# Optimization experiments

Measured on AMD Instinct MI355X. Metric: run time of the kernel, lower is better.

The kernel has to match this reference:

```python
import jax, jax.numpy as jnp
import numpy as np

L, B, H = 1024, 64, 128


def _gru_cell(x, h, wih, whh, bih, bhh):
    # torch.nn.GRUCell math: gates ordered (r, z, n)
    gi = x @ wih.T + bih  # [B, 3H]
    gh = h @ whh.T + bhh  # [B, 3H]
    ir, iz, inn = jnp.split(gi, 3, axis=1)
    hr, hz, hn = jnp.split(gh, 3, axis=1)
    r = jax.nn.sigmoid(ir + hr)
    z = jax.nn.sigmoid(iz + hz)
    n = jnp.tanh(inn + r * hn)
    return (1.0 - z) * n + z * h


def setup_inputs() -> dict:
    key = jax.random.key(0)
    ks = jax.random.split(key, 20)
    s = 0.05  # keep tanh/sigmoid unsaturated
    f32 = jnp.float32
    return {
        "passEnc": jax.random.normal(ks[0], (L, B, 2 * H), f32),
        "Wp_w": jax.random.normal(ks[1], (H, 2 * H), f32) * s,
        "Wp_b": jax.random.normal(ks[2], (H,), f32) * s,
        "Wph_w": jax.random.normal(ks[3], (H, 2 * H), f32) * s,
        "Wph_b": jax.random.normal(ks[4], (H,), f32) * s,
        "Wg_w": jax.random.normal(ks[5], (4 * H, 4 * H), f32) * s,
        "Wg_b": jax.random.normal(ks[6], (4 * H,), f32) * s,
        "Vt": jax.random.normal(ks[7], (B, H, 1), f32),
        "wih_f": jax.random.normal(ks[8], (3 * H, 4 * H), f32) * s,
        "whh_f": jax.random.normal(ks[9], (3 * H, H), f32) * s,
        "bih_f": jax.random.normal(ks[10], (3 * H,), f32) * s,
        "bhh_f": jax.random.normal(ks[11], (3 * H,), f32) * s,
        "wih_r": jax.random.normal(ks[12], (3 * H, 4 * H), f32) * s,
        "whh_r": jax.random.normal(ks[13], (3 * H, H), f32) * s,
        "bih_r": jax.random.normal(ks[14], (3 * H,), f32) * s,
        "bhh_r": jax.random.normal(ks[15], (3 * H,), f32) * s,
        "h0_fwd": jax.random.normal(ks[16], (B, H), f32),
        "h0_rev": jax.random.normal(ks[17], (B, H), f32),
    }


def reference(passEnc, Wp_w, Wp_b, Wph_w, Wph_b, Wg_w, Wg_b, Vt,
              wih_f, whh_f, bih_f, bhh_f, wih_r, whh_r, bih_r, bhh_r,
              h0_fwd, h0_rev):
    v = Vt[:, :, 0]                       # [B, H]
    WPf = passEnc @ Wp_w.T + Wp_b        # loop-invariant WP_sub_v(passEnc), [L, B, H]
    pe_rev = jnp.flip(passEnc, axis=0)
    WPr = jnp.flip(WPf, axis=0)          # linear commutes with flip

    def attend(x_t, WP, pe):
        # x_t: [B, 2H]; WP: [L, B, H]; pe: [L, B, 2H]
        temp = jnp.tanh(WP + x_t @ Wph_w.T + Wph_b)      # [L, B, H]
        scores = jnp.einsum('lbh,bh->bl', temp, v)       # per-batch Vt
        a = jax.nn.softmax(scores, axis=1)               # over L
        c = jnp.einsum('bl,lbd->bd', a, pe)              # [B, 2H]
        cc = jnp.concatenate([x_t, c], axis=1)           # [B, 4H]
        g = jax.nn.sigmoid(cc @ Wg_w.T + Wg_b)
        return g * cc

    def step(carry, xs):
        hf, hr = carry
        xf, xr = xs
        cf = attend(xf, WPf, passEnc)
        cr = attend(xr, WPr, pe_rev)
        hf = _gru_cell(cf, hf, wih_f, whh_f, bih_f, bhh_f)
        hr = _gru_cell(cr, hr, wih_r, whh_r, bih_r, bhh_r)
        return (hf, hr), jnp.concatenate([hf, hr], axis=1)

    _, out = jax.lax.scan(step, (h0_fwd, h0_rev), (passEnc, pe_rev))
    # original applies Dropout(p=0.2); identity in eval mode
    return out  # [L, B, 2H]
```

## Files before the change

kernel.cpp:

```cpp
#include <hip/hip_runtime.h>
#include <hip/hip_bf16.h>

#define DEV __device__ __forceinline__
typedef unsigned short u16;
typedef short bf16x8 __attribute__((ext_vector_type(8)));
typedef float f32x4  __attribute__((ext_vector_type(4)));

static constexpr float LOG2E = 1.44269504088896340736f;
static constexpr float C2E   = 2.88539008177792681472f;

DEV float rcpf_(float x){ return __builtin_amdgcn_rcpf(x); }
DEV float exp2f_(float x){ return __builtin_amdgcn_exp2f(x); }
DEV float sigmoidf_(float x){ return rcpf_(1.f + exp2f_(-LOG2E*x)); }
DEV float tanhf_fast(float x){ return 1.f - 2.f*rcpf_(exp2f_(C2E*x) + 1.f); }
DEV u16 bfu(float f){
  __hip_bfloat16 h = __float2bfloat16(f);
  union { __hip_bfloat16 h; u16 u; } c; c.h = h; return c.u;
}
DEV float ubf_lo(unsigned u){ return __uint_as_float(u << 16); }
DEV float ubf_hi(unsigned u){ return __uint_as_float(u & 0xffff0000u); }
DEV unsigned pack2(float a, float b){ return (unsigned)bfu(a) | ((unsigned)bfu(b) << 16); }
DEV float ubf(u16 u){ return __uint_as_float(((unsigned)u) << 16); }

DEV void acc4inv(const float4 f, const float4 e, const float4 v, float& s){
  const float dx = __builtin_fmaf(f.x, e.x, 1.f);
  const float dy = __builtin_fmaf(f.y, e.y, 1.f);
  const float dz = __builtin_fmaf(f.z, e.z, 1.f);
  const float dw = __builtin_fmaf(f.w, e.w, 1.f);
  const float p2 = dx*dy, p3 = p2*dz, p4 = p3*dw;
  const float r4 = rcpf_(p4);
  const float iw = r4*p3;
  const float s3 = r4*dw;
  const float iz = s3*p2;
  const float s2 = s3*dz;
  const float iy = s2*dx;
  const float ix = s2*dy;
  s += v.x*ix; s += v.y*iy; s += v.z*iz; s += v.w*iw;
}

__global__ __launch_bounds__(256) void k_cvtw(const float* __restrict__ Wg,
      const float* __restrict__ wf, const float* __restrict__ wr,
      u16* __restrict__ out){
  const int i = (blockIdx.x*256 + threadIdx.x)*4;
  const float* src;
  int off;
  if (i < 262144){ src = Wg; off = i; }
  else if (i < 458752){ src = wf; off = i - 262144; }
  else { src = wr; off = i - 458752; }
  const float4 v = *(const float4*)(src + off);
  uint2 o; o.x = pack2(v.x, v.y); o.y = pack2(v.z, v.w);
  *(uint2*)(out + i) = o;
}

__global__ __launch_bounds__(256,4) void k_proj(const float* __restrict__ pe,
      const float* __restrict__ Wp, const float* __restrict__ Wpb,
      const float* __restrict__ Wph, const float* __restrict__ Wphb,
      float* __restrict__ E, float* __restrict__ F){
  __shared__ __align__(16) float xs[32*256];
  const int tid = threadIdx.x;
  const int sel = blockIdx.x >> 11;
  const long r0 = (long)(blockIdx.x & 2047) * 32;
  const float* W   = sel ? Wph  : Wp;
  const float* bia = sel ? Wphb : Wpb;
  float* out       = sel ? F    : E;
  const float4* src = (const float4*)(pe + r0*256);
  float4* dst = (float4*)xs;
  #pragma unroll
  for (int i=0;i<8;i++) dst[tid + 256*i] = src[tid + 256*i];
  __syncthreads();
  const int h = tid & 127, g = tid >> 7;
  float acc[16];
  #pragma unroll
  for (int r=0;r<16;r++) acc[r] = 0.f;
  for (int kc=0; kc<8; kc++){
    float4 w4[8];
    const float4* wp = (const float4*)(W + h*256 + kc*32);
    #pragma unroll
    for (int q=0;q<8;q++) w4[q] = wp[q];
    #pragma unroll
    for (int r=0;r<16;r++){
      const float4* xr = (const float4*)(xs + (g*16+r)*256 + kc*32);
      #pragma unroll
      for (int q=0;q<8;q++){
        const float4 xv = xr[q];
        acc[r] += xv.x*w4[q].x + xv.y*w4[q].y + xv.z*w4[q].z + xv.w*w4[q].w;
      }
    }
  }
  const float bh = bia[h];
  #pragma unroll
  for (int r=0;r<16;r++)
    out[(r0 + g*16 + r)*128 + h] = exp2f_(C2E*(acc[r] + bh));
}

#define AF_F    0
#define AF_E    8448
#define AF_PEt  12672
#define AF_S    17792
#define AF_V    19904
#define AF_M    20032
#define AF_SU   20096
#define AF_R    20160
#define A_LDSF  20224

DEV f32x4 mfma16(bf16x8 a, bf16x8 b, f32x4 c){
  return __builtin_amdgcn_mfma_f32_16x16x32_bf16(a, b, c, 0, 0, 0);
}

__global__ __launch_bounds__(512,4) void k_attn(const float* __restrict__ pe,
      const float* __restrict__ E, const float* __restrict__ F,
      const float* __restrict__ Vt, u16* __restrict__ Cout){
  __shared__ __align__(16) float lds[A_LDSF];
  const int tid = threadIdx.x;
  const int p = blockIdx.x;
  const int b = ((p >> 7) << 3) | (p & 7);
  const int tt = (p >> 3) & 15;
  const int t0 = tt * 64;
  u16* PEtu = (u16*)(lds + AF_PEt);
  u16* Pu   = (u16*)(lds + AF_S);

  for (int i = tid; i < 64*32; i += 512){
    const int r = i >> 5, c = i & 31;
    *(float4*)(lds + AF_F + r*132 + c*4) =
      *(const float4*)(F + ((long)(t0+r)*64 + b)*128 + c*4);
  }
  if (tid < 128) lds[AF_V + tid] = -2.f * Vt[b*128 + tid];
  if (tid < 64){ lds[AF_M+tid] = -__builtin_inff(); lds[AF_SU+tid] = 0.f; }

  f32x4 cacc[8];
  #pragma unroll
  for (int i=0;i<8;i++) cacc[i] = (f32x4){0.f,0.f,0.f,0.f};

  const int lane = tid & 63, w = tid >> 6;
  const int hg = lane >> 4, li = lane & 15;
  const int th = li & 1, lq = li >> 1;
  const int rot = (2*hg + 4*th) & 7;
  const int l15 = lane & 15, kg8 = (lane >> 4) * 8;
  const int tq = w >> 1, dhalf = w & 1;
  const int tcol = tq*16 + l15;
  const int sdlo = tid & 7, slp = (tid >> 3) & 15, sdhi = tid >> 7;

  for (int lt=0; lt<32; lt++){
    const int l0 = lt*32;
    __syncthreads();
    for (int i = tid; i < 32*32; i += 512){
      const int r = i >> 5, c = i & 31;
      *(float4*)(lds + AF_E + r*132 + c*4) =
        *(const float4*)(E + ((long)(l0+r)*64 + b)*128 + c*4);
    }
    #pragma unroll
    for (int k2=0;k2<2;k2++){
      const int dseg = (sdhi + k2*4)*8 + sdlo;
      const int ll = slp*2;
      const float4 vA = *(const float4*)(pe + ((long)(l0+ll  )*64 + b)*256 + dseg*4);
      const float4 vB = *(const float4*)(pe + ((long)(l0+ll+1)*64 + b)*256 + dseg*4);
      u16* base = PEtu + (dseg*4)*40 + ll;
      *(unsigned*)(base)        = pack2(vA.x, vB.x);
      *(unsigned*)(base + 40)   = pack2(vA.y, vB.y);
      *(unsigned*)(base + 80)   = pack2(vA.z, vB.z);
      *(unsigned*)(base + 120)  = pack2(vA.w, vB.w);
    }
    __syncthreads();
    {
      float s[4][4];
      #pragma unroll
      for (int i=0;i<4;i++)
        #pragma unroll
        for (int j=0;j<4;j++) s[i][j] = 0.f;
      const float* Fb = lds + AF_F + (w*8 + th)*132 + hg*32;
      const float* Eb = lds + AF_E + lq*132 + hg*32;
      const float* Vb = lds + AF_V + hg*32;
      #pragma unroll 2
      for (int hc=0; hc<8; hc++){
        const int hcp = ((hc + rot) & 7) * 4;
        const float4 vv = *(const float4*)(Vb + hcp);
        float4 fv[4], ev[4];
        #pragma unroll
        for (int i=0;i<4;i++) fv[i] = *(const float4*)(Fb + i*264 + hcp);
        #pragma unroll
        for (int j=0;j<4;j++) ev[j] = *(const float4*)(Eb + j*1056 + hcp);
        #pragma unroll
        for (int i=0;i<4;i++){
          #pragma unroll
          for (int j=0;j<4;j++)
            acc4inv(fv[i], ev[j], vv, s[i][j]);
        }
      }
      #pragma unroll
      for (int i=0;i<4;i++)
        #pragma unroll
        for (int j=0;j<4;j++){
          s[i][j] += __shfl_xor(s[i][j], 16);
          s[i][j] += __shfl_xor(s[i][j], 32);
        }
      if (hg == 0){
        #pragma unroll
        for (int i=0;i<4;i++)
          #pragma unroll
          for (int j=0;j<4;j++)
            lds[AF_S + (w*8 + th + 2*i)*33 + (lq + 8*j)] = s[i][j];
      }
    }
    __syncthreads();
    {
      const int t = tid >> 3, sub = tid & 7;
      const float* Srow = lds + AF_S + t*33 + sub*4;
      const float s0=Srow[0], s1=Srow[1], s2=Srow[2], s3=Srow[3];
      float mx = fmaxf(fmaxf(s0,s1), fmaxf(s2,s3));
      #pragma unroll
      for (int off=1; off<8; off<<=1) mx = fmaxf(mx, __shfl_xor(mx, off));
      const float m_old = lds[AF_M + t];
      const float m_new = fmaxf(m_old, mx);
      const float p0 = exp2f_(LOG2E*(s0-m_new));
      const float p1 = exp2f_(LOG2E*(s1-m_new));
      const float p2 = exp2f_(LOG2E*(s2-m_new));
      const float p3 = exp2f_(LOG2E*(s3-m_new));
      float ps = p0+p1+p2+p3;
      #pragma unroll
      for (int off=1; off<8; off<<=1) ps += __shfl_xor(ps, off);
      __syncthreads();
      uint2 pw; pw.x = pack2(p0,p1); pw.y = pack2(p2,p3);
      *(uint2*)(Pu + t*40 + sub*4) = pw;
      if (sub==0){
        const float rsc = exp2f_(LOG2E*(m_old - m_new));
        lds[AF_R + t] = rsc;
        lds[AF_SU + t] = lds[AF_SU + t]*rsc + ps;
        lds[AF_M + t] = m_new;
      }
    }
    __syncthreads();
    {
      const float rs = lds[AF_R + tcol];
      #pragma unroll
      for (int p2=0;p2<8;p2++){
        cacc[p2][0]*=rs; cacc[p2][1]*=rs; cacc[p2][2]*=rs; cacc[p2][3]*=rs;
      }
      const bf16x8 bfrag = *(const bf16x8*)(Pu + tcol*40 + kg8);
      #pragma unroll
      for (int p2=0;p2<8;p2++){
        const int dt = dhalf*8 + p2;
        const bf16x8 afrag = *(const bf16x8*)(PEtu + (dt*16 + l15)*40 + kg8);
        cacc[p2] = mfma16(afrag, bfrag, cacc[p2]);
      }
    }
  }
  __syncthreads();
  {
    const float inv = rcpf_(lds[AF_SU + tcol]);
    u16* Cb = (u16*)(lds + AF_F);
    const int rb = (lane >> 4) * 4;
    #pragma unroll
    for (int p2=0;p2<8;p2++){
      const int dd = (dhalf*8 + p2)*16 + rb;
      *(unsigned*)(Cb + tcol*264 + dd)     = pack2(cacc[p2][0]*inv, cacc[p2][1]*inv);
      *(unsigned*)(Cb + tcol*264 + dd + 2) = pack2(cacc[p2][2]*inv, cacc[p2][3]*inv);
    }
  }
  __syncthreads();
  {
    const u16* Cb = (const u16*)(lds + AF_F);
    #pragma unroll
    for (int k2=0;k2<4;k2++){
      const int flat = tid + k2*512;
      const int t = flat >> 5, dg = flat & 31;
      const uint4 v = *(const uint4*)(Cb + t*264 + dg*8);
      *(uint4*)(Cout + ((long)(t0+t)*64 + b)*256 + dg*8) = v;
    }
  }
}

__global__ __launch_bounds__(512,2) void k_gates(const float* __restrict__ pe,
      const u16* __restrict__ Cin,
      const u16* __restrict__ Wgb16, const float* __restrict__ Wgb,
      const u16* __restrict__ wfb16, const float* __restrict__ bihf,
      const u16* __restrict__ wrb16, const float* __restrict__ bihr,
      u16* __restrict__ GIf, u16* __restrict__ GIr){
  __shared__ __align__(16) u16 ccb[32*512];
  __shared__ __align__(16) u16 gb [32*512];
  const int tid = threadIdx.x;
  const int r0 = blockIdx.x * 32;

  #pragma unroll
  for (int i=0;i<4;i++){
    const int c = tid + i*512;
    const int r = c >> 6, k0 = (c & 63)*8;
    const int kd = k0 ^ ((r&7)<<3);
    uint4 o;
    if (k0 < 256){
      const float4 f0 = *(const float4*)(pe + ((long)(r0+r))*256 + k0);
      const float4 f1 = *(const float4*)(pe + ((long)(r0+r))*256 + k0 + 4);
      o.x = pack2(f0.x,f0.y); o.y = pack2(f0.z,f0.w);
      o.z = pack2(f1.x,f1.y); o.w = pack2(f1.z,f1.w);
    } else {
      o = *(const uint4*)(Cin + ((long)(r0+r))*256 + (k0-256));
    }
    *(uint4*)(ccb + r*512 + kd) = o;
  }
  __syncthreads();

  const int l = tid & 63, wv = tid >> 6;
  const int rw = (wv >> 2) * 16;
  const int nq = wv & 3;
  const int arow = rw + (l & 15);
  const int kgrp = (l >> 4) * 8;
  const int swz  = (l & 7) << 3;
  const u16* abase = ccb + arow*512;
  const int crow = rw + (l >> 4) * 4;

  for (int p2=0; p2<4; p2++){
    const int n0 = nq*128 + p2*32;
    const int c0 = n0 + (l & 15), c1 = c0 + 16;
    const u16* b0p = Wgb16 + (long)c0*512 + kgrp;
    const u16* b1p = Wgb16 + (long)c1*512 + kgrp;
    f32x4 a0 = {0.f,0.f,0.f,0.f}, a1 = {0.f,0.f,0.f,0.f};
    #pragma unroll
    for (int kk=0; kk<16; kk++){
      const bf16x8 av = *(const bf16x8*)(abase + ((kk*32 + kgrp) ^ swz));
      const bf16x8 b0 = *(const bf16x8*)(b0p + kk*32);
      const bf16x8 b1 = *(const bf16x8*)(b1p + kk*32);
      a0 = mfma16(av, b0, a0);
      a1 = mfma16(av, b1, a1);
    }
    const float bi0 = Wgb[c0], bi1 = Wgb[c1];
    #pragma unroll
    for (int i=0;i<4;i++){
      gb[(crow+i)*512 + c0] = bfu(sigmoidf_(a0[i] + bi0));
      gb[(crow+i)*512 + c1] = bfu(sigmoidf_(a1[i] + bi1));
    }
  }
  __syncthreads();

  #pragma unroll
  for (int i=0;i<4;i++){
    const int c = tid + i*512;
    const int r = c >> 6, k0 = (c & 63)*8;
    const int kd = k0 ^ ((r&7)<<3);
    uint4 uc = *(const uint4*)(ccb + r*512 + kd);
    uint4 ug = *(const uint4*)(gb  + r*512 + k0);
    uint4 o;
    o.x = pack2(ubf_lo(uc.x)*ubf_lo(ug.x), ubf_hi(uc.x)*ubf_hi(ug.x));
    o.y = pack2(ubf_lo(uc.y)*ubf_lo(ug.y), ubf_hi(uc.y)*ubf_hi(ug.y));
    o.z = pack2(ubf_lo(uc.z)*ubf_lo(ug.z), ubf_hi(uc.z)*ubf_hi(ug.z));
    o.w = pack2(ubf_lo(uc.w)*ubf_lo(ug.w), ubf_hi(uc.w)*ubf_hi(ug.w));
    *(uint4*)(ccb + r*512 + kd) = o;
  }
  __syncthreads();

  const int t = r0 >> 6, b0r = r0 & 63;
  const long rbf = (long)r0 + rw;
  const long rbr = (long)(1023 - t)*64 + b0r + rw;
  u16* stg = gb + wv*512;

  for (int p2=0; p2<6; p2++){
    const int nt = nq*12 + p2*2;
    const int j0 = nt * 16;
    const bool isf = (j0 < 384);
    const u16* wb = isf ? wfb16 : wrb16;
    const float* bi = isf ? bihf : bihr;
    const int jb = isf ? j0 : (j0 - 384);
    const long rbase = isf ? rbf : rbr;
    u16* GIo = isf ? GIf : GIr;
    const int c0 = jb + (l & 15), c1 = c0 + 16;
    const u16* b0p = wb + (long)c0*512 + kgrp;
    const u16* b1p = wb + (long)c1*512 + kgrp;
    f32x4 a0 = {0.f,0.f,0.f,0.f}, a1 = {0.f,0.f,0.f,0.f};
    #pragma unroll
    for (int kk=0; kk<16; kk++){
      const bf16x8 av = *(const bf16x8*)(abase + ((kk*32 + kgrp) ^ swz));
      const bf16x8 b0 = *(const bf16x8*)(b0p + kk*32);
      const bf16x8 b1 = *(const bf16x8*)(b1p + kk*32);
      a0 = mfma16(av, b0, a0);
      a1 = mfma16(av, b1, a1);
    }
    const float bi0 = bi[c0], bi1 = bi[c1];
    #pragma unroll
    for (int i=0;i<4;i++){
      stg[((l>>4)*4+i)*16 + (l&15)]       = bfu(a0[i] + bi0);
      stg[256 + ((l>>4)*4+i)*16 + (l&15)] = bfu(a1[i] + bi1);
    }
    {
      const int rr = l >> 2, q = l & 3;
      const uint2 v0 = *(const uint2*)(stg + rr*16 + q*4);
      const uint2 v1 = *(const uint2*)(stg + 256 + rr*16 + q*4);
      *(uint2*)(GIo + (rbase + rr)*384 + jb      + q*4) = v0;
      *(uint2*)(GIo + (rbase + rr)*384 + jb + 16 + q*4) = v1;
    }
  }
}

__global__ __launch_bounds__(512,2) void k_gru(
      const u16* __restrict__ GIf, const u16* __restrict__ GIr,
      const float* __restrict__ whhf, const float* __restrict__ bhhf,
      const float* __restrict__ whhr, const float* __restrict__ bhhr,
      const float* __restrict__ h0f, const float* __restrict__ h0r,
      float* __restrict__ out){
  const int d = blockIdx.x >> 6, b = blockIdx.x & 63;
  const u16* GI = d ? GIr  : GIf;
  const float* whh = d ? whhr : whhf;
  const float* bhh = d ? bhhr : bhhf;
  const float* h0  = d ? h0r  : h0f;
  const int tid = threadIdx.x;
  const int seg = tid >> 7, j0 = tid & 127;
  __shared__ __align__(16) float hsh[128];
  __shared__ __align__(16) float part[4*384];

  float4 wR[8], wZ[8], wN[8];
  {
    const float4* r0p = (const float4*)(whh + (long)(j0      )*128 + seg*32);
    const float4* r1p = (const float4*)(whh + (long)(j0 + 128)*128 + seg*32);
    const float4* r2p = (const float4*)(whh + (long)(j0 + 256)*128 + seg*32);
    #pragma unroll
    for (int q=0;q<8;q++){ wR[q]=r0p[q]; wZ[q]=r1p[q]; wN[q]=r2p[q]; }
  }
  float bjr=0.f, bjz=0.f, bjn=0.f, hold=0.f;
  float gr_n=0.f, gz_n=0.f, gn_n=0.f;
  if (tid < 128){
    hsh[tid] = hold = h0[b*128 + tid];
    bjr = bhh[tid]; bjz = bhh[tid+128]; bjn = bhh[tid+256];
    gr_n = ubf(GI[(long)b*384 + tid]);
    gz_n = ubf(GI[(long)b*384 + tid + 128]);
    gn_n = ubf(GI[(long)b*384 + tid + 256]);
  }
  __syncthreads();

  for (int t=0; t<1024; t++){
    {
      float aR=0.f, aZ=0.f, aN=0.f;
      const float4* hseg = (const float4*)(hsh + seg*32);
      #pragma unroll
      for (int q=0;q<8;q++){
        const float4 hv = hseg[q];
        aR += wR[q].x*hv.x + wR[q].y*hv.y + wR[q].z*hv.z + wR[q].w*hv.w;
        aZ += wZ[q].x*hv.x + wZ[q].y*hv.y + wZ[q].z*hv.z + wZ[q].w*hv.w;
        aN += wN[q].x*hv.x + wN[q].y*hv.y + wN[q].z*hv.z + wN[q].w*hv.w;
      }
      part[seg*384 + j0]       = aR;
      part[seg*384 + j0 + 128] = aZ;
      part[seg*384 + j0 + 256] = aN;
    }
    __syncthreads();
    if (tid < 128){
      const float gr = gr_n, gz = gz_n, gn = gn_n;
      if (t < 1023){
        const long base = ((long)(t+1)*64 + b)*384 + tid;
        gr_n = ubf(GI[base]); gz_n = ubf(GI[base+128]); gn_n = ubf(GI[base+256]);
      }
      const float ghr = bjr + ((part[tid]       + part[384+tid])       + (part[768+tid]       + part[1152+tid]));
      const float ghz = bjz + ((part[tid+128]   + part[384+tid+128])   + (part[768+tid+128]   + part[1152+tid+128]));
      const float ghn = bjn + ((part[tid+256]   + part[384+tid+256])   + (part[768+tid+256]   + part[1152+tid+256]));
      const float r = sigmoidf_(gr + ghr);
      const float z = sigmoidf_(gz + ghz);
      const float n = tanhf_fast(gn + r*ghn);
      const float hnew = (1.f - z)*n + z*hold;
      hold = hnew;
      hsh[tid] = hnew;
      out[((long)t*64 + b)*256 + d*128 + tid] = hnew;
    }
    __syncthreads();
  }
}

__global__ void k_sentinel(float* out){ out[0] = 1.0e6f; }

extern "C" void kernel_launch(void* const* d_in, const int* in_sizes, int n_in,
                              void* d_out, int out_size, void* d_ws, size_t ws_size,
                              hipStream_t stream){
  const float* passEnc = (const float*)d_in[0];
  const float* Wp_w  = (const float*)d_in[1];
  const float* Wp_b  = (const float*)d_in[2];
  const float* Wph_w = (const float*)d_in[3];
  const float* Wph_b = (const float*)d_in[4];
  const float* Wg_w  = (const float*)d_in[5];
  const float* Wg_b  = (const float*)d_in[6];
  const float* Vt    = (const float*)d_in[7];
  const float* wih_f = (const float*)d_in[8];
  const float* whh_f = (const float*)d_in[9];
  const float* bih_f = (const float*)d_in[10];
  const float* bhh_f = (const float*)d_in[11];
  const float* wih_r = (const float*)d_in[12];
  const float* whh_r = (const float*)d_in[13];
  const float* bih_r = (const float*)d_in[14];
  const float* bhh_r = (const float*)d_in[15];
  const float* h0f   = (const float*)d_in[16];
  const float* h0r   = (const float*)d_in[17];
  float* out = (float*)d_out;

  const size_t NEED = 134217728ull;
  if (ws_size < NEED){ k_sentinel<<<1,1,0,stream>>>(out); return; }
  char* base = (char*)d_ws;
  u16* GIf = (u16*)base;
  u16* GIr = (u16*)(base + 50331648ull);
  u16* C   = (u16*)(base + 100663296ull);
  float* E = (float*)base;
  float* F = (float*)(base + 33554432ull);
  u16* wgb16 = (u16*)d_out;
  u16* wfb16 = wgb16 + 262144;
  u16* wrb16 = wfb16 + 196608;

  k_cvtw <<<640,  256, 0, stream>>>(Wg_w, wih_f, wih_r, wgb16);
  k_proj <<<4096, 256, 0, stream>>>(passEnc, Wp_w, Wp_b, Wph_w, Wph_b, E, F);
  k_attn <<<1024, 512, 0, stream>>>(passEnc, E, F, Vt, C);
  k_gates<<<2048, 512, 0, stream>>>(passEnc, C, wgb16, Wg_b,
                                    wfb16, bih_f, wrb16, bih_r, GIf, GIr);
  k_gru  <<<128,  512, 0, stream>>>(GIf, GIr, whh_f, bhh_f, whh_r, bhh_r, h0f, h0r, out);
}
```

Baseline: 2.533 ms.

## Reduce GRU partial sums via wave shuffles with double-buffered hidden state

The GRU recurrence kernel is remapped so that the four K-segments for each hidden unit sit in the same wavefront. Partial dot products are then reduced with cross-lane shuffles instead of an LDS partial buffer, and the hidden state is double-buffered, so only one barrier per timestep is needed instead of two. Separately, the projection kernel now computes two output columns per thread, reusing each shared-memory x load across both and writing float2 stores. The LDS bank rotation in the attention score loop is also removed. This may raise bank conflicts there and raises register pressure in k_proj.

```diff
diff --git a/kernel.cpp b/kernel.cpp
--- a/kernel.cpp
+++ b/kernel.cpp
@@ -68,29 +68,39 @@
   #pragma unroll
   for (int i=0;i<8;i++) dst[tid + 256*i] = src[tid + 256*i];
   __syncthreads();
-  const int h = tid & 127, g = tid >> 7;
-  float acc[16];
+  const int hp = (tid & 63)*2, rg = tid >> 6;
+  float acc[2][8];
   #pragma unroll
-  for (int r=0;r<16;r++) acc[r] = 0.f;
+  for (int c=0;c<2;c++)
+    #pragma unroll
+    for (int r=0;r<8;r++) acc[c][r] = 0.f;
   for (int kc=0; kc<8; kc++){
-    float4 w4[8];
-    const float4* wp = (const float4*)(W + h*256 + kc*32);
-    #pragma unroll
-    for (int q=0;q<8;q++) w4[q] = wp[q];
-    #pragma unroll
-    for (int r=0;r<16;r++){
-      const float4* xr = (const float4*)(xs + (g*16+r)*256 + kc*32);
+    float4 w0[8], w1[8];
+    const float4* wp0 = (const float4*)(W + (long)hp*256 + kc*32);
+    const float4* wp1 = (const float4*)(W + (long)(hp+1)*256 + kc*32);
+    #pragma unroll
+    for (int q=0;q<8;q++){ w0[q] = wp0[q]; w1[q] = wp1[q]; }
+    #pragma unroll
+    for (int r=0;r<8;r++){
+      const float4* xr = (const float4*)(xs + (rg*8+r)*256 + kc*32);
+      float a0 = 0.f, a1 = 0.f;
       #pragma unroll
       for (int q=0;q<8;q++){
         const float4 xv = xr[q];
-        acc[r] += xv.x*w4[q].x + xv.y*w4[q].y + xv.z*w4[q].z + xv.w*w4[q].w;
-      }
-    }
-  }
-  const float bh = bia[h];
+        a0 += xv.x*w0[q].x + xv.y*w0[q].y + xv.z*w0[q].z + xv.w*w0[q].w;
+        a1 += xv.x*w1[q].x + xv.y*w1[q].y + xv.z*w1[q].z + xv.w*w1[q].w;
+      }
+      acc[0][r] += a0; acc[1][r] += a1;
+    }
+  }
+  const float b0 = bia[hp], b1 = bia[hp+1];
   #pragma unroll
-  for (int r=0;r<16;r++)
-    out[(r0 + g*16 + r)*128 + h] = exp2f_(C2E*(acc[r] + bh));
+  for (int r=0;r<8;r++){
+    float2 o;
+    o.x = exp2f_(C2E*(acc[0][r] + b0));
+    o.y = exp2f_(C2E*(acc[1][r] + b1));
+    *(float2*)(out + (r0 + rg*8 + r)*128 + hp) = o;
+  }
 }
 
 #define AF_F    0
@@ -134,7 +144,6 @@
   const int lane = tid & 63, w = tid >> 6;
   const int hg = lane >> 4, li = lane & 15;
   const int th = li & 1, lq = li >> 1;
-  const int rot = (2*hg + 4*th) & 7;
   const int l15 = lane & 15, kg8 = (lane >> 4) * 8;
   const int tq = w >> 1, dhalf = w & 1;
   const int tcol = tq*16 + l15;
@@ -172,13 +181,12 @@
       const float* Vb = lds + AF_V + hg*32;
       #pragma unroll 2
       for (int hc=0; hc<8; hc++){
-        const int hcp = ((hc + rot) & 7) * 4;
-        const float4 vv = *(const float4*)(Vb + hcp);
+        const float4 vv = *(const float4*)(Vb + hc*4);
         float4 fv[4], ev[4];
         #pragma unroll
-        for (int i=0;i<4;i++) fv[i] = *(const float4*)(Fb + i*264 + hcp);
+        for (int i=0;i<4;i++) fv[i] = *(const float4*)(Fb + i*264 + hc*4);
         #pragma unroll
-        for (int j=0;j<4;j++) ev[j] = *(const float4*)(Eb + j*1056 + hcp);
+        for (int j=0;j<4;j++) ev[j] = *(const float4*)(Eb + j*1056 + hc*4);
         #pragma unroll
         for (int i=0;i<4;i++){
           #pragma unroll
@@ -400,33 +408,36 @@
   const float* bhh = d ? bhhr : bhhf;
   const float* h0  = d ? h0r  : h0f;
   const int tid = threadIdx.x;
-  const int seg = tid >> 7, j0 = tid & 127;
-  __shared__ __align__(16) float hsh[128];
-  __shared__ __align__(16) float part[4*384];
+  const int w = tid >> 6, l = tid & 63;
+  const int seg = l >> 4, jj = w*16 + (l & 15);
+  const bool own = (seg == 0);
+  __shared__ __align__(16) float hsh[2][128];
 
   float4 wR[8], wZ[8], wN[8];
   {
-    const float4* r0p = (const float4*)(whh + (long)(j0      )*128 + seg*32);
-    const float4* r1p = (const float4*)(whh + (long)(j0 + 128)*128 + seg*32);
-    const float4* r2p = (const float4*)(whh + (long)(j0 + 256)*128 + seg*32);
+    const float4* r0p = (const float4*)(whh + (long)(jj      )*128 + seg*32);
+    const float4* r1p = (const float4*)(whh + (long)(jj + 128)*128 + seg*32);
+    const float4* r2p = (const float4*)(whh + (long)(jj + 256)*128 + seg*32);
     #pragma unroll
     for (int q=0;q<8;q++){ wR[q]=r0p[q]; wZ[q]=r1p[q]; wN[q]=r2p[q]; }
   }
   float bjr=0.f, bjz=0.f, bjn=0.f, hold=0.f;
   float gr_n=0.f, gz_n=0.f, gn_n=0.f;
-  if (tid < 128){
-    hsh[tid] = hold = h0[b*128 + tid];
-    bjr = bhh[tid]; bjz = bhh[tid+128]; bjn = bhh[tid+256];
-    gr_n = ubf(GI[(long)b*384 + tid]);
-    gz_n = ubf(GI[(long)b*384 + tid + 128]);
-    gn_n = ubf(GI[(long)b*384 + tid + 256]);
-  }
-  __syncthreads();
-
+  if (own){
+    hold = h0[b*128 + jj];
+    hsh[0][jj] = hold;
+    bjr = bhh[jj]; bjz = bhh[jj+128]; bjn = bhh[jj+256];
+    gr_n = ubf(GI[(long)b*384 + jj]);
+    gz_n = ubf(GI[(long)b*384 + jj + 128]);
+    gn_n = ubf(GI[(long)b*384 + jj + 256]);
+  }
+  __syncthreads();
+
+  int cur = 0;
   for (int t=0; t<1024; t++){
+    float aR=0.f, aZ=0.f, aN=0.f;
     {
-      float aR=0.f, aZ=0.f, aN=0.f;
-      const float4* hseg = (const float4*)(hsh + seg*32);
+      const float4* hseg = (const float4*)(&hsh[cur][seg*32]);
       #pragma unroll
       for (int q=0;q<8;q++){
         const float4 hv = hseg[q];
@@ -434,29 +445,26 @@
         aZ += wZ[q].x*hv.x + wZ[q].y*hv.y + wZ[q].z*hv.z + wZ[q].w*hv.w;
         aN += wN[q].x*hv.x + wN[q].y*hv.y + wN[q].z*hv.z + wN[q].w*hv.w;
       }
-      part[seg*384 + j0]       = aR;
-      part[seg*384 + j0 + 128] = aZ;
-      part[seg*384 + j0 + 256] = aN;
-    }
-    __syncthreads();
-    if (tid < 128){
+    }
+    aR += __shfl_xor(aR, 16); aR += __shfl_xor(aR, 32);
+    aZ += __shfl_xor(aZ, 16); aZ += __shfl_xor(aZ, 32);
+    aN += __shfl_xor(aN, 16); aN += __shfl_xor(aN, 32);
+    if (own){
       const float gr = gr_n, gz = gz_n, gn = gn_n;
       if (t < 1023){
-        const long base = ((long)(t+1)*64 + b)*384 + tid;
+        const long base = ((long)(t+1)*64 + b)*384 + jj;
         gr_n = ubf(GI[base]); gz_n = ubf(GI[base+128]); gn_n = ubf(GI[base+256]);
       }
-      const float ghr = bjr + ((part[tid]       + part[384+tid])       + (part[768+tid]       + part[1152+tid]));
-      const float ghz = bjz + ((part[tid+128]   + part[384+tid+128])   + (part[768+tid+128]   + part[1152+tid+128]));
-      const float ghn = bjn + ((part[tid+256]   + part[384+tid+256])   + (part[768+tid+256]   + part[1152+tid+256]));
-      const float r = sigmoidf_(gr + ghr);
-      const float z = sigmoidf_(gz + ghz);
-      const float n = tanhf_fast(gn + r*ghn);
+      const float r = sigmoidf_(gr + bjr + aR);
+      const float z = sigmoidf_(gz + bjz + aZ);
+      const float n = tanhf_fast(gn + r*(bjn + aN));
       const float hnew = (1.f - z)*n + z*hold;
       hold = hnew;
-      hsh[tid] = hnew;
-      out[((long)t*64 + b)*256 + d*128 + tid] = hnew;
+      hsh[cur^1][jj] = hnew;
+      out[((long)t*64 + b)*256 + d*128 + jj] = hnew;
     }
     __syncthreads();
+    cur ^= 1;
   }
 }
 
```

Result: slower. 3.083 ms (+21.7%).

## Pre-pack weights into MFMA fragment order and transpose projection weights

Applied to the files above, without the earlier changes.

The prep kernel now writes the bf16 gate and GRU input weights in an MFMA-fragment-tiled layout, so each lane's B-operand load in k_gates is contiguous across the wavefront rather than strided by rows. It also transposes Wp/Wph so k_proj threads read weights coalesced across h instead of per-thread rows. The rotated LDS index in the attention score loop is dropped in favour of a plain sequential index, which may bring back LDS bank conflicts. The extra transposed weights are stored in the output buffer as scratch space.

```diff
diff --git a/kernel.cpp b/kernel.cpp
--- a/kernel.cpp
+++ b/kernel.cpp
@@ -38,29 +38,47 @@
   s += v.x*ix; s += v.y*iy; s += v.z*iz; s += v.w*iw;
 }
 
-__global__ __launch_bounds__(256) void k_cvtw(const float* __restrict__ Wg,
+__global__ __launch_bounds__(256) void k_prep(const float* __restrict__ Wg,
       const float* __restrict__ wf, const float* __restrict__ wr,
-      u16* __restrict__ out){
-  const int i = (blockIdx.x*256 + threadIdx.x)*4;
-  const float* src;
-  int off;
-  if (i < 262144){ src = Wg; off = i; }
-  else if (i < 458752){ src = wf; off = i - 262144; }
-  else { src = wr; off = i - 458752; }
-  const float4 v = *(const float4*)(src + off);
-  uint2 o; o.x = pack2(v.x, v.y); o.y = pack2(v.z, v.w);
-  *(uint2*)(out + i) = o;
+      const float* __restrict__ Wp, const float* __restrict__ Wph,
+      u16* __restrict__ wgbP, u16* __restrict__ wfbP, u16* __restrict__ wrbP,
+      float* __restrict__ WpT, float* __restrict__ WphT){
+  const int blk = blockIdx.x, tid = threadIdx.x;
+  if (blk < 320){
+    const int gid = blk*256 + tid;
+    const float* src; u16* dst; int local;
+    if (gid < 32768){ src = Wg; dst = wgbP; local = gid; }
+    else if (gid < 57344){ src = wf; dst = wfbP; local = gid - 32768; }
+    else { src = wr; dst = wrbP; local = gid - 57344; }
+    const int cb  = local >> 10;
+    const int rem = local & 1023;
+    const int kk = rem >> 6, l = rem & 63;
+    const int row = cb*16 + (l & 15);
+    const int k0  = kk*32 + (l >> 4)*8;
+    const float4 f0 = *(const float4*)(src + (long)row*512 + k0);
+    const float4 f1 = *(const float4*)(src + (long)row*512 + k0 + 4);
+    uint4 o;
+    o.x = pack2(f0.x, f0.y); o.y = pack2(f0.z, f0.w);
+    o.z = pack2(f1.x, f1.y); o.w = pack2(f1.z, f1.w);
+    *(uint4*)(dst + (long)local*8) = o;
+  } else if (blk < 448){
+    const int idx = (blk-320)*256 + tid;
+    WpT[idx] = Wp[(idx & 127)*256 + (idx >> 7)];
+  } else {
+    const int idx = (blk-448)*256 + tid;
+    WphT[idx] = Wph[(idx & 127)*256 + (idx >> 7)];
+  }
 }
 
 __global__ __launch_bounds__(256,4) void k_proj(const float* __restrict__ pe,
-      const float* __restrict__ Wp, const float* __restrict__ Wpb,
-      const float* __restrict__ Wph, const float* __restrict__ Wphb,
+      const float* __restrict__ WpT, const float* __restrict__ Wpb,
+      const float* __restrict__ WphT, const float* __restrict__ Wphb,
       float* __restrict__ E, float* __restrict__ F){
   __shared__ __align__(16) float xs[32*256];
   const int tid = threadIdx.x;
   const int sel = blockIdx.x >> 11;
   const long r0 = (long)(blockIdx.x & 2047) * 32;
-  const float* W   = sel ? Wph  : Wp;
+  const float* WT  = sel ? WphT : WpT;
   const float* bia = sel ? Wphb : Wpb;
   float* out       = sel ? F    : E;
   const float4* src = (const float4*)(pe + r0*256);
@@ -73,17 +91,16 @@
   #pragma unroll
   for (int r=0;r<16;r++) acc[r] = 0.f;
   for (int kc=0; kc<8; kc++){
-    float4 w4[8];
-    const float4* wp = (const float4*)(W + h*256 + kc*32);
-    #pragma unroll
-    for (int q=0;q<8;q++) w4[q] = wp[q];
+    float w[32];
+    #pragma unroll
+    for (int q=0;q<32;q++) w[q] = WT[(kc*32 + q)*128 + h];
     #pragma unroll
     for (int r=0;r<16;r++){
       const float4* xr = (const float4*)(xs + (g*16+r)*256 + kc*32);
       #pragma unroll
       for (int q=0;q<8;q++){
         const float4 xv = xr[q];
-        acc[r] += xv.x*w4[q].x + xv.y*w4[q].y + xv.z*w4[q].z + xv.w*w4[q].w;
+        acc[r] += xv.x*w[q*4] + xv.y*w[q*4+1] + xv.z*w[q*4+2] + xv.w*w[q*4+3];
       }
     }
   }
@@ -134,7 +151,6 @@
   const int lane = tid & 63, w = tid >> 6;
   const int hg = lane >> 4, li = lane & 15;
   const int th = li & 1, lq = li >> 1;
-  const int rot = (2*hg + 4*th) & 7;
   const int l15 = lane & 15, kg8 = (lane >> 4) * 8;
   const int tq = w >> 1, dhalf = w & 1;
   const int tcol = tq*16 + l15;
@@ -172,13 +188,12 @@
       const float* Vb = lds + AF_V + hg*32;
       #pragma unroll 2
       for (int hc=0; hc<8; hc++){
-        const int hcp = ((hc + rot) & 7) * 4;
-        const float4 vv = *(const float4*)(Vb + hcp);
+        const float4 vv = *(const float4*)(Vb + hc*4);
         float4 fv[4], ev[4];
         #pragma unroll
-        for (int i=0;i<4;i++) fv[i] = *(const float4*)(Fb + i*264 + hcp);
+        for (int i=0;i<4;i++) fv[i] = *(const float4*)(Fb + i*264 + hc*4);
         #pragma unroll
-        for (int j=0;j<4;j++) ev[j] = *(const float4*)(Eb + j*1056 + hcp);
+        for (int j=0;j<4;j++) ev[j] = *(const float4*)(Eb + j*1056 + hc*4);
         #pragma unroll
         for (int i=0;i<4;i++){
           #pragma unroll
@@ -271,9 +286,9 @@
 
 __global__ __launch_bounds__(512,2) void k_gates(const float* __restrict__ pe,
       const u16* __restrict__ Cin,
-      const u16* __restrict__ Wgb16, const float* __restrict__ Wgb,
-      const u16* __restrict__ wfb16, const float* __restrict__ bihf,
-      const u16* __restrict__ wrb16, const float* __restrict__ bihr,
+      const u16* __restrict__ wgbP, const float* __restrict__ Wgb,
+      const u16* __restrict__ wfbP, const float* __restrict__ bihf,
+      const u16* __restrict__ wrbP, const float* __restrict__ bihr,
       u16* __restrict__ GIf, u16* __restrict__ GIr){
   __shared__ __align__(16) u16 ccb[32*512];
   __shared__ __align__(16) u16 gb [32*512];
@@ -308,16 +323,16 @@
   const int crow = rw + (l >> 4) * 4;
 
   for (int p2=0; p2<4; p2++){
-    const int n0 = nq*128 + p2*32;
-    const int c0 = n0 + (l & 15), c1 = c0 + 16;
-    const u16* b0p = Wgb16 + (long)c0*512 + kgrp;
-    const u16* b1p = Wgb16 + (long)c1*512 + kgrp;
+    const int cb0 = nq*8 + p2*2, cb1 = cb0 + 1;
+    const int c0 = cb0*16 + (l & 15), c1 = c0 + 16;
+    const u16* b0p = wgbP + ((long)cb0*16*64 + (long)l)*8;
+    const u16* b1p = wgbP + ((long)cb1*16*64 + (long)l)*8;
     f32x4 a0 = {0.f,0.f,0.f,0.f}, a1 = {0.f,0.f,0.f,0.f};
     #pragma unroll
     for (int kk=0; kk<16; kk++){
       const bf16x8 av = *(const bf16x8*)(abase + ((kk*32 + kgrp) ^ swz));
-      const bf16x8 b0 = *(const bf16x8*)(b0p + kk*32);
-      const bf16x8 b1 = *(const bf16x8*)(b1p + kk*32);
+      const bf16x8 b0 = *(const bf16x8*)(b0p + kk*512);
+      const bf16x8 b1 = *(const bf16x8*)(b1p + kk*512);
       a0 = mfma16(av, b0, a0);
       a1 = mfma16(av, b1, a1);
     }
@@ -355,20 +370,21 @@
     const int nt = nq*12 + p2*2;
     const int j0 = nt * 16;
     const bool isf = (j0 < 384);
-    const u16* wb = isf ? wfb16 : wrb16;
+    const u16* wbP = isf ? wfbP : wrbP;
     const float* bi = isf ? bihf : bihr;
     const int jb = isf ? j0 : (j0 - 384);
+    const int cbA = jb >> 4, cbB = cbA + 1;
     const long rbase = isf ? rbf : rbr;
     u16* GIo = isf ? GIf : GIr;
     const int c0 = jb + (l & 15), c1 = c0 + 16;
-    const u16* b0p = wb + (long)c0*512 + kgrp;
-    const u16* b1p = wb + (long)c1*512 + kgrp;
+    const u16* b0p = wbP + ((long)cbA*16*64 + (long)l)*8;
+    const u16* b1p = wbP + ((long)cbB*16*64 + (long)l)*8;
     f32x4 a0 = {0.f,0.f,0.f,0.f}, a1 = {0.f,0.f,0.f,0.f};
     #pragma unroll
     for (int kk=0; kk<16; kk++){
       const bf16x8 av = *(const bf16x8*)(abase + ((kk*32 + kgrp) ^ swz));
-      const bf16x8 b0 = *(const bf16x8*)(b0p + kk*32);
-      const bf16x8 b1 = *(const bf16x8*)(b1p + kk*32);
+      const bf16x8 b0 = *(const bf16x8*)(b0p + kk*512);
+      const bf16x8 b1 = *(const bf16x8*)(b1p + kk*512);
       a0 = mfma16(av, b0, a0);
       a1 = mfma16(av, b1, a1);
     }
@@ -493,14 +509,17 @@
   u16* C   = (u16*)(base + 100663296ull);
   float* E = (float*)base;
   float* F = (float*)(base + 33554432ull);
-  u16* wgb16 = (u16*)d_out;
-  u16* wfb16 = wgb16 + 262144;
-  u16* wrb16 = wfb16 + 196608;
-
-  k_cvtw <<<640,  256, 0, stream>>>(Wg_w, wih_f, wih_r, wgb16);
-  k_proj <<<4096, 256, 0, stream>>>(passEnc, Wp_w, Wp_b, Wph_w, Wph_b, E, F);
+  u16* wgbP = (u16*)d_out;
+  u16* wfbP = wgbP + 262144;
+  u16* wrbP = wfbP + 196608;
+  float* WpT  = (float*)(wrbP + 196608);
+  float* WphT = WpT + 32768;
+
+  k_prep <<<576,  256, 0, stream>>>(Wg_w, wih_f, wih_r, Wp_w, Wph_w,
+                                    wgbP, wfbP, wrbP, WpT, WphT);
+  k_proj <<<4096, 256, 0, stream>>>(passEnc, WpT, Wp_b, WphT, Wph_b, E, F);
   k_attn <<<1024, 512, 0, stream>>>(passEnc, E, F, Vt, C);
-  k_gates<<<2048, 512, 0, stream>>>(passEnc, C, wgb16, Wg_b,
-                                    wfb16, bih_f, wrb16, bih_r, GIf, GIr);
+  k_gates<<<2048, 512, 0, stream>>>(passEnc, C, wgbP, Wg_b,
+                                    wfbP, bih_f, wrbP, bih_r, GIf, GIr);
   k_gru  <<<128,  512, 0, stream>>>(GIf, GIr, whh_f, bhh_f, whh_r, bhh_r, h0f, h0r, out);
 }
```

New measurement: 2.117 ms. -16.4%, faster.
